# Kernel tuning notes

Hardware: AMD Instinct MI355X
Metric: run time of the kernel (lower is better)

Reference implementation:

```python
import jax, jax.numpy as jnp
import numpy as np

T_TYPES = 3
IN_DIM = 128
HID = 128
B = 8192
N_ALLY = 15
N_OPP = 16
N_NODES = 1 + N_ALLY + N_OPP


def setup_inputs() -> dict:
    key = jax.random.key(0)
    k1, k2, k3, k4 = jax.random.split(key, 4)
    h = jax.random.normal(k1, (B, N_NODES, IN_DIM), dtype=jnp.float32)
    ALL_TYPE_MASK = jax.random.bernoulli(k2, 0.4, (T_TYPES, B, N_NODES))
    # learned params (xavier-ish scale)
    W = jax.random.normal(k3, (T_TYPES, IN_DIM, HID), dtype=jnp.float32) * 0.1
    a = jax.random.normal(k4, (T_TYPES, 2 * HID, 1), dtype=jnp.float32) * 0.1
    return {"h": h, "ALL_TYPE_MASK": ALL_TYPE_MASK, "num_ally": N_ALLY,
            "num_opp": N_OPP, "self_type": 0, "W": W, "a": a}


def _het_gat(h, ALL_TYPE_MASK, num_ally, num_opp, W, a):
    T, hid = W.shape[0], W.shape[-1]
    mask_self = ALL_TYPE_MASK[:, :, 0]                       # (T,B) True -> this type's W used for self
    mask_ally = ALL_TYPE_MASK[:, :, 1:1 + num_ally]          # (T,B,Na)
    mask_opp = ALL_TYPE_MASK[:, :, 1 + num_ally:]            # (T,B,No)
    h_self = h[:, 0, :]                                      # (B,D)
    h_ally = h[:, 1:1 + num_ally, :]                         # (B,Na,D)
    h_opp = h[:, 1 + num_ally:, :]                           # (B,No,D)
    # per-type projections (the original loops over types; batched einsum here)
    H_SELF = jnp.einsum('bd,tdh->tbh', h_self, W)            # (T,B,H)
    H_ALLY = jnp.einsum('bnd,tdh->tbnh', h_ally, W)          # (T,B,Na,H)
    H_OPP = jnp.einsum('bnd,tdh->tbnh', h_opp, W)            # (T,B,No,H)
    a_top = a[:, :hid, 0]                                    # (T,H) acts on self part
    a_bot = a[:, hid:, 0]                                    # (T,H) acts on neighbor part

    def att_sum(H_nb, mask_nb):
        # score e[b,i,j,n] = [H_SELF[i,b] ; H_nb[j,b,n]] @ a[j]
        # decomposed dot avoids materializing the (T,T,B,N,2H) concat tensor
        s_self = jnp.einsum('ibh,jh->ijb', H_SELF, a_top)    # (T,T,B)
        s_nb = jnp.einsum('jbnh,jh->jbn', H_nb, a_bot)       # (T,B,N)
        e = s_self[:, :, :, None] + s_nb[None, :, :, :]      # (T,T,B,N) axes i,j,b,n
        m = jnp.broadcast_to(mask_nb[None], e.shape)         # mask indexed by (j,b,n), bcast over i
        Bb = e.shape[2]
        e_flat = jnp.transpose(e, (2, 0, 1, 3)).reshape(Bb, -1)   # (B, T*T*N)
        m_flat = jnp.transpose(m, (2, 0, 1, 3)).reshape(Bb, -1)
        neg_inf = jnp.asarray(-jnp.inf, e_flat.dtype)
        attn = jax.nn.softmax(jnp.where(m_flat, neg_inf, e_flat), axis=-1)
        attn = jnp.where(m_flat, jnp.zeros((), attn.dtype), attn)
        attn4 = attn.reshape(Bb, T, T, -1)                   # (B,i,j,n)
        # weighted sum over flattened (i,j,n) of H_nb[j,b,n]
        return jnp.einsum('bijn,jbnh->bh', attn4, H_nb)      # (B,H)

    ally_ws = att_sum(H_ALLY, mask_ally)
    opp_ws = att_sum(H_OPP, mask_opp)
    h_self_sum = jnp.einsum('tbh,tb->bh', H_SELF, mask_self.astype(H_SELF.dtype))
    return jax.nn.elu(h_self_sum + ally_ws + opp_ws)         # (B,H)


def reference(h, ALL_TYPE_MASK, num_ally, num_opp, self_type, W, a):
    return _het_gat(h, ALL_TYPE_MASK, num_ally, num_opp, W, a)
```

## Files before the change

kernel.cpp:

```cpp
#include <hip/hip_runtime.h>
#include <math.h>

#define NB 8192
#define G 4
#define NBLK (NB / G)
#define NNODES 32
#define TT 3
#define DIM 128
#define HID 128
#define USTR 132

__global__ __launch_bounds__(128) void gat_prep(
    const float* __restrict__ Wg,
    const float* __restrict__ ag,
    float* __restrict__ uv)
{
    int e = blockIdx.x, d = threadIdx.x;
    int wi, aoff;
    if (e < 9) { wi = e / 3; aoff = (e % 3) * 2 * HID; }
    else       { wi = e - 9; aoff = wi * 2 * HID + HID; }
    const float* wrow = Wg + wi * DIM * HID + d * HID;
    const float* arow = ag + aoff;
    float acc = 0.f;
    #pragma unroll 16
    for (int h = 0; h < HID; ++h) acc += wrow[h] * arow[h];
    uv[e * DIM + d] = acc;
}

__device__ __forceinline__ int swz_slot(int n, int c) { return n * 32 + (c ^ (n & 7)); }

__device__ __forceinline__ void lds_barrier() {
    asm volatile("s_waitcnt lgkmcnt(0)" ::: "memory");
    __builtin_amdgcn_s_barrier();
}

__device__ __forceinline__ void stage_row(const float* __restrict__ hrow,
                                          float* lbuf, int tid) {
    const int wv = tid >> 6, lane = tid & 63;
    #pragma unroll
    for (int k = 0; k < 4; ++k) {
        int s = wv * 256 + k * 64 + lane;
        int n = s >> 5, c = s & 31;
        const float4* g = (const float4*)hrow + (n * 32 + (c ^ (n & 7)));
        float4* l = (float4*)lbuf + (wv * 256 + k * 64);
        __builtin_amdgcn_global_load_lds(
            (const __attribute__((address_space(1))) void*)g,
            (__attribute__((address_space(3))) void*)l, 16, 0, 0);
    }
}

__global__ __launch_bounds__(256, 4) void gat_main(
    const float* __restrict__ hg,
    const int* __restrict__ maskg,
    const float* __restrict__ Wg,
    const float* __restrict__ uv,
    float* __restrict__ outg)
{
    __shared__ __align__(16) float hL[2 * NNODES * DIM];
    __shared__ __align__(16) float uvL[12 * USTR];
    __shared__ float sTop[16];
    __shared__ float sNb[TT * NNODES];
    __shared__ unsigned char mvB[G * 96];

    const int tid = threadIdx.x;
    const int b0 = blockIdx.x * G;
    const int dq = tid & 3;

    #pragma unroll
    for (int k = 0; k < 6; ++k) {
        int i = tid + k * 256;
        uvL[(i >> 7) * USTR + (i & 127)] = uv[i];
    }
    if (tid < 96) {
        int t = tid >> 5, node = tid & 31;
        #pragma unroll
        for (int g = 0; g < G; ++g)
            mvB[g * 96 + tid] = (unsigned char)(
                maskg[(size_t)t * NB * NNODES + (size_t)(b0 + g) * NNODES + node] ? 1 : 0);
    }

    stage_row(hg + (size_t)b0 * (NNODES * DIM), hL, tid);
    __syncthreads();

    float gr[G][TT];

    #pragma unroll
    for (int g = 0; g < G; ++g) {
        const float* hb = hL + (g & 1) * (NNODES * DIM);

        if (g + 1 < G)
            stage_row(hg + (size_t)(b0 + g + 1) * (NNODES * DIM),
                      hL + ((g + 1) & 1) * (NNODES * DIM), tid);

        if (tid < 228) {
            const float4* hb4 = (const float4*)hb;
            if (tid < 192) {
                int task4 = tid >> 2;
                int t  = task4 >> 4;
                int n0 = (task4 & 15) * 2;
                const float4* up = (const float4*)&uvL[(9 + t) * USTR];
                float a0 = 0.f, a1 = 0.f;
                #pragma unroll
                for (int k = 0; k < 8; ++k) {
                    int c = dq + 4 * k;
                    float4 x0 = hb4[swz_slot(n0,     c)];
                    float4 x1 = hb4[swz_slot(n0 + 1, c)];
                    float4 u  = up[c];
                    a0 += x0.x*u.x + x0.y*u.y + x0.z*u.z + x0.w*u.w;
                    a1 += x1.x*u.x + x1.y*u.y + x1.z*u.z + x1.w*u.w;
                }
                a0 += __shfl_xor(a0, 1, 64); a0 += __shfl_xor(a0, 2, 64);
                a1 += __shfl_xor(a1, 1, 64); a1 += __shfl_xor(a1, 2, 64);
                if (dq == 0) { sNb[t * 32 + n0] = a0; sNb[t * 32 + n0 + 1] = a1; }
            } else {
                int e = (tid - 192) >> 2;
                const float4* up = (const float4*)&uvL[e * USTR];
                float a = 0.f;
                #pragma unroll
                for (int k = 0; k < 8; ++k) {
                    int c = dq + 4 * k;
                    float4 x = hb4[c];
                    float4 u = up[c];
                    a += x.x*u.x + x.y*u.y + x.z*u.z + x.w*u.w;
                }
                a += __shfl_xor(a, 1, 64); a += __shfl_xor(a, 2, 64);
                if (dq == 0) sTop[e] = a;
            }
        }
        lds_barrier();

        int wv = tid >> 6;
        if (wv == 0) {
            int lane = tid;
            bool act = lane < 45;
            int j = act ? lane / 15 : 0;
            int n = act ? lane % 15 : 0;
            int mk = 1; float sv = 0.f;
            if (act) {
                mk = mvB[g * 96 + j * 32 + 1 + n];
                sv = sNb[j * 32 + 1 + n];
            }
            float e0 = sTop[0 + j] + sv;
            float e1 = sTop[3 + j] + sv;
            float e2 = sTop[6 + j] + sv;
            bool live = act && (mk == 0);
            float lm = live ? fmaxf(e0, fmaxf(e1, e2)) : -__builtin_inff();
            #pragma unroll
            for (int off = 32; off; off >>= 1) lm = fmaxf(lm, __shfl_xor(lm, off, 64));
            float es = live ? (expf(e0 - lm) + expf(e1 - lm) + expf(e2 - lm)) : 0.f;
            float Z = es;
            #pragma unroll
            for (int off = 32; off; off >>= 1) Z += __shfl_xor(Z, off, 64);
            float w = (live && Z > 0.f) ? es / Z : 0.f;
            if (act) sNb[j * 32 + 1 + n] = w;
        } else if (wv == 1) {
            int lane = tid - 64;
            bool act = lane < 48;
            int j = act ? (lane >> 4) : 0;
            int n = act ? (lane & 15) : 0;
            int mk = 1; float sv = 0.f;
            if (act) {
                mk = mvB[g * 96 + j * 32 + 16 + n];
                sv = sNb[j * 32 + 16 + n];
            }
            float e0 = sTop[0 + j] + sv;
            float e1 = sTop[3 + j] + sv;
            float e2 = sTop[6 + j] + sv;
            bool live = act && (mk == 0);
            float lm = live ? fmaxf(e0, fmaxf(e1, e2)) : -__builtin_inff();
            #pragma unroll
            for (int off = 32; off; off >>= 1) lm = fmaxf(lm, __shfl_xor(lm, off, 64));
            float es = live ? (expf(e0 - lm) + expf(e1 - lm) + expf(e2 - lm)) : 0.f;
            float Z = es;
            #pragma unroll
            for (int off = 32; off; off >>= 1) Z += __shfl_xor(Z, off, 64);
            float w = (live && Z > 0.f) ? es / Z : 0.f;
            if (act) sNb[j * 32 + 16 + n] = w;
        } else if (wv == 2) {
            int lane = tid - 128;
            if (lane < 3)
                sNb[lane * 32 + 0] = mvB[g * 96 + lane * 32 + 0] ? 1.f : 0.f;
        }
        lds_barrier();

        if (tid < 128) {
            int d = tid;
            int chi = d >> 2, clo = d & 3;
            float a0 = 0.f, a1 = 0.f, a2 = 0.f;
            #pragma unroll
            for (int n = 0; n < NNODES; ++n) {
                float hv = hb[n * DIM + ((chi ^ (n & 7)) << 2) + clo];
                a0 += sNb[n] * hv;
                a1 += sNb[NNODES + n] * hv;
                a2 += sNb[2 * NNODES + n] * hv;
            }
            gr[g][0] = a0; gr[g][1] = a1; gr[g][2] = a2;
        }

        asm volatile("s_waitcnt vmcnt(0) lgkmcnt(0)" ::: "memory");
        __builtin_amdgcn_s_barrier();
    }

    if (tid < 128) {
        #pragma unroll
        for (int g = 0; g < G; ++g) {
            hL[g * 384 + 0 * 128 + tid] = gr[g][0];
            hL[g * 384 + 1 * 128 + tid] = gr[g][1];
            hL[g * 384 + 2 * 128 + tid] = gr[g][2];
        }
    }
    __syncthreads();

    {
        int hq  = tid & 31;
        int dq8 = tid >> 5;
        float4 acc[G];
        #pragma unroll
        for (int g = 0; g < G; ++g) acc[g] = make_float4(0.f, 0.f, 0.f, 0.f);
        #pragma unroll
        for (int t = 0; t < TT; ++t) {
            const float* wbase = Wg + ((size_t)t * DIM + dq8 * 16) * HID + 4 * hq;
            const float* gbase = &hL[t * 128 + dq8 * 16];
            #pragma unroll 4
            for (int dd = 0; dd < 16; ++dd) {
                float4 wq = *(const float4*)(wbase + dd * HID);
                #pragma unroll
                for (int g = 0; g < G; ++g) {
                    float gv = gbase[g * 384 + dd];
                    acc[g].x += gv * wq.x;
                    acc[g].y += gv * wq.y;
                    acc[g].z += gv * wq.z;
                    acc[g].w += gv * wq.w;
                }
            }
        }
        float* pL = hL + 2048;
        #pragma unroll
        for (int g = 0; g < G; ++g)
            *(float4*)&pL[(dq8 * G + g) * DIM + 4 * hq] = acc[g];
    }
    __syncthreads();

    #pragma unroll
    for (int r = 0; r < 2; ++r) {
        int idx = tid + r * 256;
        int g = idx >> 7, h = idx & 127;
        const float* pL = hL + 2048;
        float s = 0.f;
        #pragma unroll
        for (int p = 0; p < 8; ++p) s += pL[p * 512 + idx];
        float rr = (s > 0.f) ? s : expm1f(s);
        outg[(size_t)(b0 + g) * DIM + h] = rr;
    }
}

extern "C" void kernel_launch(void* const* d_in, const int* in_sizes, int n_in,
                              void* d_out, int out_size, void* d_ws, size_t ws_size,
                              hipStream_t stream) {
    const float* hg    = (const float*)d_in[0];
    const int*   maskg = (const int*)d_in[1];
    const float* Wg    = (const float*)d_in[5];
    const float* ag    = (const float*)d_in[6];
    float* uv = (float*)d_ws;
    float* outg = (float*)d_out;

    gat_prep<<<12, 128, 0, stream>>>(Wg, ag, uv);
    gat_main<<<NBLK, 256, 0, stream>>>(hg, maskg, Wg, uv, outg);
}
```

Measured before the change: 227.2 us.

## Vectorize attention-weighted sum and projection with float4 LDS layouts

Stores attention weights node-major (one float4 of per-type weights per node), so the weighted-sum step reads one float4 of h per node. Each group of 4 threads splits the nodes and combines partial sums with shuffles. The W projection now reads the per-type aggregates as float4 and loads four W rows per step, and the final reduction plus ELU is done as float4 by 128 threads. The aim is fewer LDS instructions and wider global stores. In exchange it adds shuffle reductions and leaves some threads idle.

```diff
diff --git a/kernel.cpp b/kernel.cpp
--- a/kernel.cpp
+++ b/kernel.cpp
@@ -59,7 +59,7 @@
     __shared__ __align__(16) float hL[2 * NNODES * DIM];
     __shared__ __align__(16) float uvL[12 * USTR];
     __shared__ float sTop[16];
-    __shared__ float sNb[TT * NNODES];
+    __shared__ __align__(16) float sNbT[NNODES * 4];
     __shared__ unsigned char mvB[G * 96];
 
     const int tid = threadIdx.x;
@@ -82,7 +82,7 @@
     stage_row(hg + (size_t)b0 * (NNODES * DIM), hL, tid);
     __syncthreads();
 
-    float gr[G][TT];
+    float4 grq[G];
 
     #pragma unroll
     for (int g = 0; g < G; ++g) {
@@ -111,7 +111,7 @@
                 }
                 a0 += __shfl_xor(a0, 1, 64); a0 += __shfl_xor(a0, 2, 64);
                 a1 += __shfl_xor(a1, 1, 64); a1 += __shfl_xor(a1, 2, 64);
-                if (dq == 0) { sNb[t * 32 + n0] = a0; sNb[t * 32 + n0 + 1] = a1; }
+                if (dq == 0) { sNbT[n0 * 4 + t] = a0; sNbT[(n0 + 1) * 4 + t] = a1; }
             } else {
                 int e = (tid - 192) >> 2;
                 const float4* up = (const float4*)&uvL[e * USTR];
@@ -138,7 +138,7 @@
             int mk = 1; float sv = 0.f;
             if (act) {
                 mk = mvB[g * 96 + j * 32 + 1 + n];
-                sv = sNb[j * 32 + 1 + n];
+                sv = sNbT[(1 + n) * 4 + j];
             }
             float e0 = sTop[0 + j] + sv;
             float e1 = sTop[3 + j] + sv;
@@ -152,7 +152,7 @@
             #pragma unroll
             for (int off = 32; off; off >>= 1) Z += __shfl_xor(Z, off, 64);
             float w = (live && Z > 0.f) ? es / Z : 0.f;
-            if (act) sNb[j * 32 + 1 + n] = w;
+            if (act) sNbT[(1 + n) * 4 + j] = w;
         } else if (wv == 1) {
             int lane = tid - 64;
             bool act = lane < 48;
@@ -161,7 +161,7 @@
             int mk = 1; float sv = 0.f;
             if (act) {
                 mk = mvB[g * 96 + j * 32 + 16 + n];
-                sv = sNb[j * 32 + 16 + n];
+                sv = sNbT[(16 + n) * 4 + j];
             }
             float e0 = sTop[0 + j] + sv;
             float e1 = sTop[3 + j] + sv;
@@ -175,82 +175,102 @@
             #pragma unroll
             for (int off = 32; off; off >>= 1) Z += __shfl_xor(Z, off, 64);
             float w = (live && Z > 0.f) ? es / Z : 0.f;
-            if (act) sNb[j * 32 + 16 + n] = w;
+            if (act) sNbT[(16 + n) * 4 + j] = w;
         } else if (wv == 2) {
             int lane = tid - 128;
             if (lane < 3)
-                sNb[lane * 32 + 0] = mvB[g * 96 + lane * 32 + 0] ? 1.f : 0.f;
+                sNbT[0 * 4 + lane] = mvB[g * 96 + lane * 32 + 0] ? 1.f : 0.f;
         }
         lds_barrier();
 
         if (tid < 128) {
-            int d = tid;
-            int chi = d >> 2, clo = d & 3;
-            float a0 = 0.f, a1 = 0.f, a2 = 0.f;
-            #pragma unroll
-            for (int n = 0; n < NNODES; ++n) {
-                float hv = hb[n * DIM + ((chi ^ (n & 7)) << 2) + clo];
-                a0 += sNb[n] * hv;
-                a1 += sNb[NNODES + n] * hv;
-                a2 += sNb[2 * NNODES + n] * hv;
-            }
-            gr[g][0] = a0; gr[g][1] = a1; gr[g][2] = a2;
+            int q = tid >> 2;
+            int sub = tid & 3;
+            const float4* hb4 = (const float4*)hb;
+            const float4* wq4 = (const float4*)sNbT;
+            float4 A0 = make_float4(0.f, 0.f, 0.f, 0.f);
+            float4 A1 = make_float4(0.f, 0.f, 0.f, 0.f);
+            float4 A2 = make_float4(0.f, 0.f, 0.f, 0.f);
+            #pragma unroll
+            for (int i = 0; i < 8; ++i) {
+                int n = sub + 4 * i;
+                float4 hv = hb4[swz_slot(n, q)];
+                float4 w  = wq4[n];
+                A0.x += w.x * hv.x; A0.y += w.x * hv.y; A0.z += w.x * hv.z; A0.w += w.x * hv.w;
+                A1.x += w.y * hv.x; A1.y += w.y * hv.y; A1.z += w.y * hv.z; A1.w += w.y * hv.w;
+                A2.x += w.z * hv.x; A2.y += w.z * hv.y; A2.z += w.z * hv.z; A2.w += w.z * hv.w;
+            }
+            #pragma unroll
+            for (int off = 1; off <= 2; off <<= 1) {
+                A0.x += __shfl_xor(A0.x, off, 64); A0.y += __shfl_xor(A0.y, off, 64);
+                A0.z += __shfl_xor(A0.z, off, 64); A0.w += __shfl_xor(A0.w, off, 64);
+                A1.x += __shfl_xor(A1.x, off, 64); A1.y += __shfl_xor(A1.y, off, 64);
+                A1.z += __shfl_xor(A1.z, off, 64); A1.w += __shfl_xor(A1.w, off, 64);
+                A2.x += __shfl_xor(A2.x, off, 64); A2.y += __shfl_xor(A2.y, off, 64);
+                A2.z += __shfl_xor(A2.z, off, 64); A2.w += __shfl_xor(A2.w, off, 64);
+            }
+            grq[g] = (sub == 1) ? A1 : ((sub == 2) ? A2 : A0);
         }
 
         asm volatile("s_waitcnt vmcnt(0) lgkmcnt(0)" ::: "memory");
         __builtin_amdgcn_s_barrier();
     }
 
-    if (tid < 128) {
-        #pragma unroll
-        for (int g = 0; g < G; ++g) {
-            hL[g * 384 + 0 * 128 + tid] = gr[g][0];
-            hL[g * 384 + 1 * 128 + tid] = gr[g][1];
-            hL[g * 384 + 2 * 128 + tid] = gr[g][2];
-        }
+    if (tid < 128 && (tid & 3) < 3) {
+        int q = tid >> 2, t = tid & 3;
+        #pragma unroll
+        for (int g = 0; g < G; ++g)
+            ((float4*)hL)[g * 96 + t * 32 + q] = grq[g];
     }
     __syncthreads();
 
     {
         int hq  = tid & 31;
         int dq8 = tid >> 5;
+        const float4* gA4 = (const float4*)hL;
         float4 acc[G];
         #pragma unroll
         for (int g = 0; g < G; ++g) acc[g] = make_float4(0.f, 0.f, 0.f, 0.f);
         #pragma unroll
         for (int t = 0; t < TT; ++t) {
-            const float* wbase = Wg + ((size_t)t * DIM + dq8 * 16) * HID + 4 * hq;
-            const float* gbase = &hL[t * 128 + dq8 * 16];
-            #pragma unroll 4
-            for (int dd = 0; dd < 16; ++dd) {
-                float4 wq = *(const float4*)(wbase + dd * HID);
+            const float4* wb = (const float4*)(Wg + ((size_t)t * DIM + dq8 * 16) * HID) + hq;
+            #pragma unroll
+            for (int dp = 0; dp < 4; ++dp) {
+                float4 w0 = wb[(dp * 4 + 0) * 32];
+                float4 w1 = wb[(dp * 4 + 1) * 32];
+                float4 w2 = wb[(dp * 4 + 2) * 32];
+                float4 w3 = wb[(dp * 4 + 3) * 32];
                 #pragma unroll
                 for (int g = 0; g < G; ++g) {
-                    float gv = gbase[g * 384 + dd];
-                    acc[g].x += gv * wq.x;
-                    acc[g].y += gv * wq.y;
-                    acc[g].z += gv * wq.z;
-                    acc[g].w += gv * wq.w;
+                    float4 gv = gA4[g * 96 + t * 32 + dq8 * 4 + dp];
+                    acc[g].x += gv.x * w0.x + gv.y * w1.x + gv.z * w2.x + gv.w * w3.x;
+                    acc[g].y += gv.x * w0.y + gv.y * w1.y + gv.z * w2.y + gv.w * w3.y;
+                    acc[g].z += gv.x * w0.z + gv.y * w1.z + gv.z * w2.z + gv.w * w3.z;
+                    acc[g].w += gv.x * w0.w + gv.y * w1.w + gv.z * w2.w + gv.w * w3.w;
                 }
             }
         }
-        float* pL = hL + 2048;
+        float4* pL4 = (float4*)(hL + 2048);
         #pragma unroll
         for (int g = 0; g < G; ++g)
-            *(float4*)&pL[(dq8 * G + g) * DIM + 4 * hq] = acc[g];
+            pL4[(dq8 * 4 + g) * 32 + hq] = acc[g];
     }
     __syncthreads();
 
-    #pragma unroll
-    for (int r = 0; r < 2; ++r) {
-        int idx = tid + r * 256;
-        int g = idx >> 7, h = idx & 127;
-        const float* pL = hL + 2048;
-        float s = 0.f;
-        #pragma unroll
-        for (int p = 0; p < 8; ++p) s += pL[p * 512 + idx];
-        float rr = (s > 0.f) ? s : expm1f(s);
-        outg[(size_t)(b0 + g) * DIM + h] = rr;
+    if (tid < 128) {
+        int g = tid >> 5, q = tid & 31;
+        const float4* pL4 = (const float4*)(hL + 2048);
+        float4 s = make_float4(0.f, 0.f, 0.f, 0.f);
+        #pragma unroll
+        for (int p = 0; p < 8; ++p) {
+            float4 v = pL4[p * 128 + g * 32 + q];
+            s.x += v.x; s.y += v.y; s.z += v.z; s.w += v.w;
+        }
+        s.x = (s.x > 0.f) ? s.x : expm1f(s.x);
+        s.y = (s.y > 0.f) ? s.y : expm1f(s.y);
+        s.z = (s.z > 0.f) ? s.z : expm1f(s.z);
+        s.w = (s.w > 0.f) ? s.w : expm1f(s.w);
+        ((float4*)outg)[(size_t)(b0 + g) * 32 + q] = s;
     }
 }
 
```

Measured after the change: 282.2 us. 24.2% more time.

## Single-buffer h staging, overlay LDS arena and bit-pack masks

Applied to the files above, without the earlier changes.

Replaces the double-buffered h row staging with a single buffer that is loaded and waited on at the start of each group iteration. The uv and partial-sum regions are overlaid in one LDS arena, and the per-node byte masks become one 32-bit word per type per row, loaded as int4. LDS per block drops from roughly 38 KB to about 23 KB, which lets more blocks fit per CU. The cost is that the global-to-LDS prefetch no longer overlaps compute within a block, so latency hiding now depends on running more resident blocks.

```diff
diff --git a/kernel.cpp b/kernel.cpp
--- a/kernel.cpp
+++ b/kernel.cpp
@@ -8,7 +8,6 @@
 #define TT 3
 #define DIM 128
 #define HID 128
-#define USTR 132
 
 __global__ __launch_bounds__(128) void gat_prep(
     const float* __restrict__ Wg,
@@ -33,6 +32,10 @@
     asm volatile("s_waitcnt lgkmcnt(0)" ::: "memory");
     __builtin_amdgcn_s_barrier();
 }
+__device__ __forceinline__ void vm_barrier() {
+    asm volatile("s_waitcnt vmcnt(0)" ::: "memory");
+    __builtin_amdgcn_s_barrier();
+}
 
 __device__ __forceinline__ void stage_row(const float* __restrict__ hrow,
                                           float* lbuf, int tid) {
@@ -56,49 +59,53 @@
     const float* __restrict__ uv,
     float* __restrict__ outg)
 {
-    __shared__ __align__(16) float hL[2 * NNODES * DIM];
-    __shared__ __align__(16) float uvL[12 * USTR];
+    __shared__ __align__(16) float arena[5632];
     __shared__ float sTop[16];
     __shared__ float sNb[TT * NNODES];
-    __shared__ unsigned char mvB[G * 96];
+    __shared__ unsigned int mvW[G * TT];
 
     const int tid = threadIdx.x;
     const int b0 = blockIdx.x * G;
     const int dq = tid & 3;
+    float* hL  = arena;
+    float* uvL = arena + 4096;
 
     #pragma unroll
     for (int k = 0; k < 6; ++k) {
         int i = tid + k * 256;
-        uvL[(i >> 7) * USTR + (i & 127)] = uv[i];
-    }
-    if (tid < 96) {
-        int t = tid >> 5, node = tid & 31;
-        #pragma unroll
-        for (int g = 0; g < G; ++g)
-            mvB[g * 96 + tid] = (unsigned char)(
-                maskg[(size_t)t * NB * NNODES + (size_t)(b0 + g) * NNODES + node] ? 1 : 0);
-    }
-
-    stage_row(hg + (size_t)b0 * (NNODES * DIM), hL, tid);
+        uvL[i] = uv[i];
+    }
+    if (tid < G * TT) {
+        int g = tid / TT, t = tid % TT;
+        const int4* m4 = (const int4*)(maskg + (size_t)t * NB * NNODES
+                                             + (size_t)(b0 + g) * NNODES);
+        unsigned int m = 0;
+        #pragma unroll
+        for (int q = 0; q < 8; ++q) {
+            int4 v = m4[q];
+            m |= (v.x ? 1u : 0u) << (4 * q + 0);
+            m |= (v.y ? 1u : 0u) << (4 * q + 1);
+            m |= (v.z ? 1u : 0u) << (4 * q + 2);
+            m |= (v.w ? 1u : 0u) << (4 * q + 3);
+        }
+        mvW[g * TT + t] = m;
+    }
     __syncthreads();
 
     float gr[G][TT];
 
     #pragma unroll
     for (int g = 0; g < G; ++g) {
-        const float* hb = hL + (g & 1) * (NNODES * DIM);
-
-        if (g + 1 < G)
-            stage_row(hg + (size_t)(b0 + g + 1) * (NNODES * DIM),
-                      hL + ((g + 1) & 1) * (NNODES * DIM), tid);
+        stage_row(hg + (size_t)(b0 + g) * (NNODES * DIM), hL, tid);
+        vm_barrier();
 
         if (tid < 228) {
-            const float4* hb4 = (const float4*)hb;
+            const float4* hb4 = (const float4*)hL;
             if (tid < 192) {
                 int task4 = tid >> 2;
                 int t  = task4 >> 4;
                 int n0 = (task4 & 15) * 2;
-                const float4* up = (const float4*)&uvL[(9 + t) * USTR];
+                const float4* up = (const float4*)(uvL + (9 + t) * DIM);
                 float a0 = 0.f, a1 = 0.f;
                 #pragma unroll
                 for (int k = 0; k < 8; ++k) {
@@ -114,7 +121,7 @@
                 if (dq == 0) { sNb[t * 32 + n0] = a0; sNb[t * 32 + n0 + 1] = a1; }
             } else {
                 int e = (tid - 192) >> 2;
-                const float4* up = (const float4*)&uvL[e * USTR];
+                const float4* up = (const float4*)(uvL + e * DIM);
                 float a = 0.f;
                 #pragma unroll
                 for (int k = 0; k < 8; ++k) {
@@ -135,9 +142,9 @@
             bool act = lane < 45;
             int j = act ? lane / 15 : 0;
             int n = act ? lane % 15 : 0;
-            int mk = 1; float sv = 0.f;
+            unsigned int mk = 1; float sv = 0.f;
             if (act) {
-                mk = mvB[g * 96 + j * 32 + 1 + n];
+                mk = (mvW[g * TT + j] >> (1 + n)) & 1u;
                 sv = sNb[j * 32 + 1 + n];
             }
             float e0 = sTop[0 + j] + sv;
@@ -158,9 +165,9 @@
             bool act = lane < 48;
             int j = act ? (lane >> 4) : 0;
             int n = act ? (lane & 15) : 0;
-            int mk = 1; float sv = 0.f;
+            unsigned int mk = 1; float sv = 0.f;
             if (act) {
-                mk = mvB[g * 96 + j * 32 + 16 + n];
+                mk = (mvW[g * TT + j] >> (16 + n)) & 1u;
                 sv = sNb[j * 32 + 16 + n];
             }
             float e0 = sTop[0 + j] + sv;
@@ -179,7 +186,7 @@
         } else if (wv == 2) {
             int lane = tid - 128;
             if (lane < 3)
-                sNb[lane * 32 + 0] = mvB[g * 96 + lane * 32 + 0] ? 1.f : 0.f;
+                sNb[lane * 32 + 0] = (mvW[g * TT + lane] & 1u) ? 1.f : 0.f;
         }
         lds_barrier();
 
@@ -189,24 +196,22 @@
             float a0 = 0.f, a1 = 0.f, a2 = 0.f;
             #pragma unroll
             for (int n = 0; n < NNODES; ++n) {
-                float hv = hb[n * DIM + ((chi ^ (n & 7)) << 2) + clo];
+                float hv = hL[n * DIM + ((chi ^ (n & 7)) << 2) + clo];
                 a0 += sNb[n] * hv;
                 a1 += sNb[NNODES + n] * hv;
                 a2 += sNb[2 * NNODES + n] * hv;
             }
             gr[g][0] = a0; gr[g][1] = a1; gr[g][2] = a2;
         }
-
-        asm volatile("s_waitcnt vmcnt(0) lgkmcnt(0)" ::: "memory");
-        __builtin_amdgcn_s_barrier();
+        lds_barrier();
     }
 
     if (tid < 128) {
         #pragma unroll
         for (int g = 0; g < G; ++g) {
-            hL[g * 384 + 0 * 128 + tid] = gr[g][0];
-            hL[g * 384 + 1 * 128 + tid] = gr[g][1];
-            hL[g * 384 + 2 * 128 + tid] = gr[g][2];
+            arena[g * 384 + 0 * 128 + tid] = gr[g][0];
+            arena[g * 384 + 1 * 128 + tid] = gr[g][1];
+            arena[g * 384 + 2 * 128 + tid] = gr[g][2];
         }
     }
     __syncthreads();
@@ -220,7 +225,7 @@
         #pragma unroll
         for (int t = 0; t < TT; ++t) {
             const float* wbase = Wg + ((size_t)t * DIM + dq8 * 16) * HID + 4 * hq;
-            const float* gbase = &hL[t * 128 + dq8 * 16];
+            const float* gbase = arena + t * 128 + dq8 * 16;
             #pragma unroll 4
             for (int dd = 0; dd < 16; ++dd) {
                 float4 wq = *(const float4*)(wbase + dd * HID);
@@ -234,7 +239,7 @@
                 }
             }
         }
-        float* pL = hL + 2048;
+        float* pL = arena + 1536;
         #pragma unroll
         for (int g = 0; g < G; ++g)
             *(float4*)&pL[(dq8 * G + g) * DIM + 4 * hq] = acc[g];
@@ -245,7 +250,7 @@
     for (int r = 0; r < 2; ++r) {
         int idx = tid + r * 256;
         int g = idx >> 7, h = idx & 127;
-        const float* pL = hL + 2048;
+        const float* pL = arena + 1536;
         float s = 0.f;
         #pragma unroll
         for (int p = 0; p < 8; ++p) s += pL[p * 512 + idx];
```

New measurement: 227.4 us. About the same (+0.1%).
